# Kernel tuning notes

Measured on AMD Instinct MI355X. Metric: run time of the kernel, lower is better.

Reference implementation:

```python
import jax, jax.numpy as jnp
import numpy as np

WINDOW_SIZE = 11
SIGMA = 1.5
MAX_VAL = 1.0


def _gaussian_kernel2d(ws: int, sigma: float) -> jnp.ndarray:
    # matches kornia gaussian_t: x = arange(ws) - ws//2, normalized 1D, outer product
    x = jnp.arange(ws, dtype=jnp.float32) - ws // 2
    g = jnp.exp(-(x * x) / (2.0 * sigma * sigma))
    g = g / g.sum()
    return jnp.outer(g, g)  # (ws, ws)


def _filter2d(x: jnp.ndarray, kernel: jnp.ndarray) -> jnp.ndarray:
    # depthwise 'same' conv with reflect padding, matching kornia filter2d
    B, C, H, W = x.shape
    kh, kw = kernel.shape
    pad_h = ((kh - 1) // 2, (kh - 1) - (kh - 1) // 2)
    pad_w = ((kw - 1) // 2, (kw - 1) - (kw - 1) // 2)
    xp = jnp.pad(x, ((0, 0), (0, 0), pad_h, pad_w), mode='reflect')
    k = jnp.broadcast_to(kernel[None, None], (C, 1, kh, kw)).astype(x.dtype)
    return jax.lax.conv_general_dilated(
        xp, k, window_strides=(1, 1), padding='VALID',
        dimension_numbers=('NCHW', 'OIHW', 'NCHW'), feature_group_count=C)


def setup_inputs() -> dict:
    key = jax.random.key(0)
    k1, k2 = jax.random.split(key)
    img1 = jax.random.uniform(k1, (16, 3, 512, 512), dtype=jnp.float32)
    img2 = jax.random.uniform(k2, (16, 3, 512, 512), dtype=jnp.float32)
    kernel = _gaussian_kernel2d(WINDOW_SIZE, SIGMA)  # fixed gaussian window (11,11)
    return {"img1": img1, "img2": img2, "kernel": kernel}


def reference(img1, img2, kernel):
    C1 = (0.01 * MAX_VAL) ** 2
    C2 = (0.03 * MAX_VAL) ** 2
    mu1 = _filter2d(img1, kernel)
    mu2 = _filter2d(img2, kernel)
    mu1_sq = mu1 * mu1
    mu2_sq = mu2 * mu2
    mu1_mu2 = mu1 * mu2
    sigma1_sq = _filter2d(img1 * img1, kernel) - mu1_sq
    sigma2_sq = _filter2d(img2 * img2, kernel) - mu2_sq
    sigma12 = _filter2d(img1 * img2, kernel) - mu1_mu2
    num = (2.0 * mu1_mu2 + C1) * (2.0 * sigma12 + C2)
    den = (mu1_sq + mu2_sq + C1) * (sigma1_sq + sigma2_sq + C2)
    return num / den  # (B, C, H, W) SSIM map ('same' padding -> no crop)
```

## Files before the change

kernel.cpp:

```cpp
#include <hip/hip_runtime.h>

namespace {

typedef __attribute__((ext_vector_type(2))) float f32x2;
typedef __attribute__((ext_vector_type(4))) float f32x4;

constexpr int Hd = 512, Wd = 512;
constexpr int TH = 32;
constexpr int R  = 4;
constexpr int NCH = TH / R;
constexpr int RAD = 5, WS = 11;
constexpr int SPAN = 131;
constexpr int RSTR = 4 * SPAN;
constexpr float C1c = 1e-4f;
constexpr float C2c = 9e-4f;

__device__ __forceinline__ float rcp_fast(float x) { return __builtin_amdgcn_rcpf(x); }
__device__ __forceinline__ float sgpr_f(float x) {
    return __int_as_float(__builtin_amdgcn_readfirstlane(__float_as_int(x)));
}
__device__ __forceinline__ constexpr int sw(int e) { return (e & 3) * SPAN + (e >> 2); }

__global__ __launch_bounds__(512, 6) void ssim_map_kernel(
    const float* __restrict__ img1,
    const float* __restrict__ img2,
    const float* __restrict__ kern,
    float* __restrict__ out)
{
    __shared__ __align__(16) f32x4 hb[R * RSTR];

    const int tid  = threadIdx.x;
    const int c    = tid;
    const int row0 = blockIdx.x * TH;
    const long pbase = (long)blockIdx.y * (long)(Hd * Wd);

    float g[WS];
    {
        float s = 0.f;
#pragma unroll
        for (int j = 0; j < WS; ++j) s += kern[RAD * WS + j];
        const float inv = 1.0f / s;
#pragma unroll
        for (int j = 0; j < WS; ++j) g[j] = sgpr_f(kern[RAD * WS + j] * inv);
    }

    const int wmain = sw(c + RAD);
    int whalo = -1;
    if (c >= 1 && c <= RAD) whalo = sw(RAD - c);
    else if (c >= Wd - 1 - RAD && c <= Wd - 2) whalo = sw(RAD + 1022 - c);

    f32x2 aM[WS];
    f32x2 aQ[WS];
#pragma unroll
    for (int i = 0; i < WS; ++i) {
        aM[i].x = 0.f; aM[i].y = 0.f;
        aQ[i].x = 0.f; aQ[i].y = 0.f;
    }

#pragma unroll
    for (int j = 0; j < 2 * RAD; ++j) {
        int gr = row0 - RAD + j;
        gr = (gr < 0) ? -gr : gr;
        gr = (gr >= Hd) ? (2 * Hd - 2 - gr) : gr;
        const long off = pbase + (long)gr * Wd + c;
        const float a = img1[off];
        const float b = img2[off];
        f32x2 sd; sd.x = a + b; sd.y = a - b;
        const f32x2 qq = sd * sd;
#pragma unroll
        for (int k = 0; k < WS; ++k) {
            if (k <= j) {
                const int slot = (j - k) % WS;
                f32x2 w2; w2.x = g[k]; w2.y = g[k];
                aM[slot] = __builtin_elementwise_fma(w2, sd, aM[slot]);
                aQ[slot] = __builtin_elementwise_fma(w2, qq, aQ[slot]);
            }
        }
    }

    const int hr = tid >> 7;
    const int hu = tid & 127;

#pragma unroll
    for (int ch = 0; ch < NCH; ++ch) {
        __syncthreads();

#pragma unroll
        for (int i = 0; i < R; ++i) {
            const int o = ch * R + i;
            const int j = o + 2 * RAD;
            int gr = row0 - RAD + j;
            gr = (gr < 0) ? -gr : gr;
            gr = (gr >= Hd) ? (2 * Hd - 2 - gr) : gr;
            const long off = pbase + (long)gr * Wd + c;
            const float a = img1[off];
            const float b = img2[off];
            f32x2 sd; sd.x = a + b; sd.y = a - b;
            const f32x2 qq = sd * sd;
#pragma unroll
            for (int k = 0; k < WS; ++k) {
                const int slot = (j - k) % WS;
                f32x2 w2; w2.x = g[k]; w2.y = g[k];
                aM[slot] = __builtin_elementwise_fma(w2, sd, aM[slot]);
                aQ[slot] = __builtin_elementwise_fma(w2, qq, aQ[slot]);
            }
            const int es = o % WS;
            f32x4 e;
            e.x = aM[es].x; e.y = aM[es].y;
            e.z = aQ[es].x; e.w = aQ[es].y;
            hb[i * RSTR + wmain] = e;
            if (whalo >= 0) hb[i * RSTR + whalo] = e;
            aM[es].x = 0.f; aM[es].y = 0.f;
            aQ[es].x = 0.f; aQ[es].y = 0.f;
        }

        __syncthreads();

        f32x2 hm[4], hq[4];
#pragma unroll
        for (int j = 0; j < 4; ++j) {
            hm[j].x = 0.f; hm[j].y = 0.f;
            hq[j].x = 0.f; hq[j].y = 0.f;
        }
        const f32x4* base = &hb[hr * RSTR + hu];
#pragma unroll
        for (int t = 0; t < 14; ++t) {
            const f32x4 ft = base[(t & 3) * SPAN + (t >> 2)];
            f32x2 fm; fm.x = ft.x; fm.y = ft.y;
            f32x2 fq; fq.x = ft.z; fq.y = ft.w;
#pragma unroll
            for (int j = 0; j < 4; ++j) {
                const int k = t - j;
                if (k >= 0 && k < WS) {
                    f32x2 w2; w2.x = g[k]; w2.y = g[k];
                    hm[j] = __builtin_elementwise_fma(w2, fm, hm[j]);
                    hq[j] = __builtin_elementwise_fma(w2, fq, hq[j]);
                }
            }
        }

        float rr[4];
#pragma unroll
        for (int j = 0; j < 4; ++j) {
            const f32x2 m = hm[j];
            const f32x2 q = hq[j];
            const f32x2 msq = m * m;
            const float t1 = msq.x - msq.y;
            const float t2 = msq.x + msq.y;
            const float q1 = q.x - q.y;
            const float q2 = q.x + q.y;
            const float num = fmaf(0.5f, t1, C1c) * fmaf(0.5f, q1 - t1, C2c);
            const float den = fmaf(0.5f, t2, C1c) * fmaf(0.5f, q2 - t2, C2c);
            rr[j] = num * rcp_fast(den);
        }
        f32x4 res; res.x = rr[0]; res.y = rr[1]; res.z = rr[2]; res.w = rr[3];
        f32x4* po = (f32x4*)&out[pbase + (long)(row0 + ch * R + hr) * Wd + 4 * hu];
        *po = res;
    }
}

}

extern "C" void kernel_launch(void* const* d_in, const int* in_sizes, int n_in,
                              void* d_out, int out_size, void* d_ws, size_t ws_size,
                              hipStream_t stream) {
    const float* img1 = (const float*)d_in[0];
    const float* img2 = (const float*)d_in[1];
    const float* kern = (const float*)d_in[2];
    float* outp = (float*)d_out;
    dim3 grid(Hd / TH, 48);
    ssim_map_kernel<<<grid, dim3(512), 0, stream>>>(img1, img2, kern, outp);
}
```

Before: 153.6 us.

## Double-buffer LDS and prefetch rows two chunks ahead to overlap loads

Splits the shared horizontal buffer in two so the vertical pass for chunk ch+1 writes one buffer while the horizontal pass reads chunk ch from the other, which removes one barrier per chunk. Global row loads are issued two chunks ahead into register buffers to hide memory latency. In exchange it doubles LDS use, adds registers for the prefetch buffers, and lowers the launch-bounds occupancy hint from 6 to 4 blocks per CU.

```diff
diff --git a/kernel.cpp b/kernel.cpp
--- a/kernel.cpp
+++ b/kernel.cpp
@@ -21,13 +21,50 @@
 }
 __device__ __forceinline__ constexpr int sw(int e) { return (e & 3) * SPAN + (e >> 2); }
 
-__global__ __launch_bounds__(512, 6) void ssim_map_kernel(
+
+#define VPHASE(CH, PA, PB, BUF)                                         \
+    _Pragma("unroll")                                                   \
+    for (int i = 0; i < R; ++i) {                                       \
+        const int o = (CH) * R + i;                                     \
+        const int j = o + 2 * RAD;                                      \
+        const float a = (PA)[i];                                        \
+        const float b = (PB)[i];                                        \
+        f32x2 sd; sd.x = a + b; sd.y = a - b;                           \
+        const f32x2 qq = sd * sd;                                       \
+        _Pragma("unroll")                                               \
+        for (int k = 0; k < WS; ++k) {                                  \
+            const int slot = (j - k) % WS;     \
+            f32x2 w2; w2.x = g[k]; w2.y = g[k];                         \
+            aM[slot] = __builtin_elementwise_fma(w2, sd, aM[slot]);     \
+            aQ[slot] = __builtin_elementwise_fma(w2, qq, aQ[slot]);     \
+        }                                                               \
+        const int es = o % WS;                                          \
+        f32x4 e;                                                        \
+        e.x = aM[es].x; e.y = aM[es].y;                                 \
+        e.z = aQ[es].x; e.w = aQ[es].y;                                 \
+        (BUF)[i * RSTR + wmain] = e;                                    \
+        if (whalo >= 0) (BUF)[i * RSTR + whalo] = e;                    \
+        aM[es].x = 0.f; aM[es].y = 0.f;                                 \
+        aQ[es].x = 0.f; aQ[es].y = 0.f;                                 \
+    }
+
+#define PREFETCH(CHUNK, PA, PB)                                         \
+    _Pragma("unroll")                                                   \
+    for (int i = 0; i < R; ++i) {                                       \
+        int gr = row0 + RAD + (CHUNK) * R + i;                          \
+        gr = (gr >= Hd) ? (2 * Hd - 2 - gr) : gr;                       \
+        const long off = pbase + (long)gr * Wd + c;                     \
+        (PA)[i] = img1[off];                                            \
+        (PB)[i] = img2[off];                                            \
+    }
+
+__global__ __launch_bounds__(512, 4) void ssim_map_kernel(
     const float* __restrict__ img1,
     const float* __restrict__ img2,
     const float* __restrict__ kern,
     float* __restrict__ out)
 {
-    __shared__ __align__(16) f32x4 hb[R * RSTR];
+    __shared__ __align__(16) f32x4 hb[2][R * RSTR];
 
     const int tid  = threadIdx.x;
     const int c    = tid;
@@ -78,6 +115,12 @@
         }
     }
 
+    float plaA[R], plbA[R], plaB[R], plbB[R];
+    PREFETCH(0, plaA, plbA)
+    PREFETCH(1, plaB, plbB)
+
+    VPHASE(0, plaA, plbA, (&hb[0][0]))
+
     const int hr = tid >> 7;
     const int hu = tid & 127;
 
@@ -85,36 +128,10 @@
     for (int ch = 0; ch < NCH; ++ch) {
         __syncthreads();
 
-#pragma unroll
-        for (int i = 0; i < R; ++i) {
-            const int o = ch * R + i;
-            const int j = o + 2 * RAD;
-            int gr = row0 - RAD + j;
-            gr = (gr < 0) ? -gr : gr;
-            gr = (gr >= Hd) ? (2 * Hd - 2 - gr) : gr;
-            const long off = pbase + (long)gr * Wd + c;
-            const float a = img1[off];
-            const float b = img2[off];
-            f32x2 sd; sd.x = a + b; sd.y = a - b;
-            const f32x2 qq = sd * sd;
-#pragma unroll
-            for (int k = 0; k < WS; ++k) {
-                const int slot = (j - k) % WS;
-                f32x2 w2; w2.x = g[k]; w2.y = g[k];
-                aM[slot] = __builtin_elementwise_fma(w2, sd, aM[slot]);
-                aQ[slot] = __builtin_elementwise_fma(w2, qq, aQ[slot]);
-            }
-            const int es = o % WS;
-            f32x4 e;
-            e.x = aM[es].x; e.y = aM[es].y;
-            e.z = aQ[es].x; e.w = aQ[es].y;
-            hb[i * RSTR + wmain] = e;
-            if (whalo >= 0) hb[i * RSTR + whalo] = e;
-            aM[es].x = 0.f; aM[es].y = 0.f;
-            aQ[es].x = 0.f; aQ[es].y = 0.f;
+        if (ch + 2 < NCH) {
+            if ((ch & 1) == 0) { PREFETCH(ch + 2, plaA, plbA) }
+            else               { PREFETCH(ch + 2, plaB, plbB) }
         }
-
-        __syncthreads();
 
         f32x2 hm[4], hq[4];
 #pragma unroll
@@ -122,7 +139,7 @@
             hm[j].x = 0.f; hm[j].y = 0.f;
             hq[j].x = 0.f; hq[j].y = 0.f;
         }
-        const f32x4* base = &hb[hr * RSTR + hu];
+        const f32x4* base = &hb[ch & 1][hr * RSTR + hu];
 #pragma unroll
         for (int t = 0; t < 14; ++t) {
             const f32x4 ft = base[(t & 3) * SPAN + (t >> 2)];
@@ -156,8 +173,16 @@
         f32x4 res; res.x = rr[0]; res.y = rr[1]; res.z = rr[2]; res.w = rr[3];
         f32x4* po = (f32x4*)&out[pbase + (long)(row0 + ch * R + hr) * Wd + 4 * hu];
         *po = res;
+
+        if (ch + 1 < NCH) {
+            if (((ch + 1) & 1) == 0) { VPHASE(ch + 1, plaA, plbA, (&hb[0][0])) }
+            else                      { VPHASE(ch + 1, plaB, plbB, (&hb[1][0])) }
+        }
     }
 }
+
+#undef VPHASE
+#undef PREFETCH
 
 }
 
```

New measurement: 144.9 us. 5.6% less time.
